# Kernel optimization log

Hardware: AMD Instinct MI355X
Metric: run time of the kernel (lower is better)

Reference implementation:

```python
import jax, jax.numpy as jnp
import numpy as np

N_RNA, N_DIS = 40000, 3000
E_EDGES, T = 600000, 10000
RNA_IN, D_FEAT, HID, EXP_D = 512, 256, 512, 256
N_EXP, HEADS = 8, 8
HD = HID // HEADS          # per-head dim inside HANConv
MHA_HD = EXP_D // HEADS    # per-head dim in cross-attention
FUSION = 2 * HID


def setup_inputs() -> dict:
    key = jax.random.key(0)
    ks = iter(jax.random.split(key, 48))
    def nrm(shape, s=0.02):
        return jax.random.normal(next(ks), shape, dtype=jnp.float32) * s
    inp = {
        "x_rna": jax.random.normal(next(ks), (N_RNA, RNA_IN), dtype=jnp.float32),
        "x_dis": jax.random.normal(next(ks), (N_DIS, D_FEAT), dtype=jnp.float32),
        "Wd": nrm((RNA_IN, D_FEAT)), "bd": jnp.zeros((RNA_IN,), jnp.float32),
        "Wp_r": nrm((HID, RNA_IN)), "bp_r": jnp.zeros((HID,), jnp.float32),
        "Wp_d": nrm((HID, RNA_IN)), "bp_d": jnp.zeros((HID,), jnp.float32),
        "a_src_rd": nrm((HEADS, HD), 0.1), "a_dst_rd": nrm((HEADS, HD), 0.1),
        "a_src_dr": nrm((HEADS, HD), 0.1), "a_dst_dr": nrm((HEADS, HD), 0.1),
        "kW": nrm((HID, HID)), "kb": jnp.zeros((HID,), jnp.float32),
        "qv": nrm((HID,), 0.1),
        "Wl": nrm((HID, HID)), "bl": jnp.zeros((HID,), jnp.float32),
        "W_exp": nrm((N_EXP, FUSION, EXP_D)), "b_exp": jnp.zeros((N_EXP, EXP_D), jnp.float32),
        "W_gate": nrm((4, HID, N_EXP)),
        "W_head": nrm((4, 2 * EXP_D, EXP_D)), "b_head": jnp.zeros((4, EXP_D), jnp.float32),
        "in_w": nrm((3 * EXP_D, EXP_D)), "in_b": jnp.zeros((3 * EXP_D,), jnp.float32),
        "out_w": nrm((EXP_D, EXP_D)), "out_b": jnp.zeros((EXP_D,), jnp.float32),
        "Wdp": nrm((EXP_D, HID)), "bdp": jnp.zeros((EXP_D,), jnp.float32),
        "ei_rd_src": jax.random.randint(next(ks), (E_EDGES,), 0, N_RNA),
        "ei_rd_dst": jax.random.randint(next(ks), (E_EDGES,), 0, N_DIS),
        "ei_dr_src": jax.random.randint(next(ks), (E_EDGES,), 0, N_DIS),
        "ei_dr_dst": jax.random.randint(next(ks), (E_EDGES,), 0, N_RNA),
        "idx_rels": jax.random.randint(next(ks), (4, T), 0, N_RNA),
    }
    return inp


def _han_edge(x_src, x_dst, ei_src, ei_dst, a_src, a_dst, n_dst):
    # x_*: [N, H, D]; GAT-style attention with softmax per destination node (PyG HANConv edge step)
    as_ = (x_src * a_src).sum(-1)                                 # [Ns, H]
    ad_ = (x_dst * a_dst).sum(-1)                                 # [Nd, H]
    alpha = jax.nn.leaky_relu(as_[ei_src] + ad_[ei_dst], 0.2)     # [E, H]
    amax = jax.ops.segment_max(alpha, ei_dst, num_segments=n_dst)
    ex = jnp.exp(alpha - amax[ei_dst])
    den = jax.ops.segment_sum(ex, ei_dst, num_segments=n_dst)
    w = ex / (den[ei_dst] + 1e-16)
    msg = x_src[ei_src] * w[:, :, None]                           # [E, H, D]
    out = jax.ops.segment_sum(msg, ei_dst, num_segments=n_dst)    # [Nd, H, D]
    return jax.nn.relu(out.reshape(n_dst, -1))


def _semantic(outs, kW, kb, qv):
    # outs: [M, N, F]; metapath-level (semantic) attention from HANConv
    s = (jnp.tanh(outs @ kW.T + kb).mean(axis=1) * qv).sum(-1)    # [M]
    beta = jax.nn.softmax(s)
    return (beta[:, None, None] * outs).sum(0)


def reference(x_rna, x_dis, Wd, bd, Wp_r, bp_r, Wp_d, bp_d,
              a_src_rd, a_dst_rd, a_src_dr, a_dst_dr,
              kW, kb, qv, Wl, bl, W_exp, b_exp, W_gate, W_head, b_head,
              in_w, in_b, out_w, out_b, Wdp, bdp,
              ei_rd_src, ei_rd_dst, ei_dr_src, ei_dr_dst, idx_rels):
    # ---- HAN encoder ----
    xd = x_dis @ Wd.T + bd                                        # disease feat -> rna_in_dim
    hr0 = (x_rna @ Wp_r.T + bp_r).reshape(N_RNA, HEADS, HD)
    hd0 = (xd @ Wp_d.T + bp_d).reshape(N_DIS, HEADS, HD)
    out_dis = _han_edge(hr0, hd0, ei_rd_src, ei_rd_dst, a_src_rd, a_dst_rd, N_DIS)
    out_rna = _han_edge(hd0, hr0, ei_dr_src, ei_dr_dst, a_src_dr, a_dst_dr, N_RNA)
    h_rna = _semantic(out_rna[None], kW, kb, qv) @ Wl.T + bl      # shared final lin
    h_dis = _semantic(out_dis[None], kW, kb, qv) @ Wl.T + bl
    # ---- MoE with per-relation gating ----
    d_global = h_dis.mean(axis=0)
    fusion = jnp.concatenate([h_rna, jnp.broadcast_to(d_global, h_rna.shape)], axis=1)  # [N, 2H]
    E = jax.nn.relu(jnp.einsum('nf,efd->ned', fusion, W_exp) + b_exp)  # [N, Nexp, Ed]
    h_t = h_rna[idx_rels]                                         # [4, T, H]
    scores = jnp.einsum('rth,rhe->rte', h_t, W_gate)              # raw gate scores (no softmax)
    u = (E[idx_rels] * scores[..., None]).sum(axis=2)             # [4, T, Ed]
    U = u.mean(axis=1)                                            # [4, Ed]
    # ---- cross attention over 4 task tokens ----
    qkv = U @ in_w.T + in_b
    q, k, v = jnp.split(qkv, 3, axis=-1)
    def heads(z):
        return z.reshape(4, HEADS, MHA_HD).transpose(1, 0, 2)     # [H, 4, dh]
    qh, kh, vh = heads(q), heads(k), heads(v)
    attn = jax.nn.softmax(jnp.einsum('htd,hsd->hts', qh, kh) / np.float32(np.sqrt(MHA_HD)), axis=-1)
    o = jnp.einsum('hts,hsd->htd', attn, vh).transpose(1, 0, 2).reshape(4, EXP_D)
    U_prime = o @ out_w.T + out_b                                 # [4, Ed]
    # ---- per-relation heads and disease scores ----
    cross = jnp.broadcast_to(U_prime[:, None, :], u.shape)
    cat = jnp.concatenate([u, cross], axis=-1)                    # [4, T, 2Ed]
    p = jax.nn.relu(jnp.einsum('rtc,rcd->rtd', cat, W_head) + b_head[:, None, :])
    d_proj = h_dis @ Wdp.T + bdp                                  # [Ndis, Ed]
    return jax.nn.sigmoid(jnp.einsum('rtd,md->rtm', p, d_proj))   # [4, T, Ndis]
```

## Files before the change

### kernel.cpp

```cpp
#include <hip/hip_runtime.h>
#include <math.h>

constexpr int NRNA = 40000;
constexpr int NDIS = 3000;
constexpr int NEDG = 600000;
constexpr int TREL = 10000;

typedef __attribute__((ext_vector_type(8))) short bh8;
typedef __attribute__((ext_vector_type(4))) float f32x4;

__device__ inline float bf2f(ushort x) {
    union { uint u; float f; } v; v.u = ((uint)x) << 16; return v.f;
}
__device__ inline ushort f2bf(float f) {
    union { float f; uint u; } v; v.f = f;
    uint u = v.u;
    uint r = (u + 0x7fffu + ((u >> 16) & 1u)) >> 16;
    return (ushort)r;
}
__device__ inline float bflo(uint w) { union { uint u; float f; } v; v.u = w << 16; return v.f; }
__device__ inline float bfhi(uint w) { union { uint u; float f; } v; v.u = w & 0xffff0000u; return v.f; }

__device__ inline void gload16(const ushort* g, ushort* l) {
    __builtin_amdgcn_global_load_lds(
        (const __attribute__((address_space(1))) unsigned int*)(const void*)g,
        (__attribute__((address_space(3))) unsigned int*)(void*)l, 16, 0, 0);
}

__device__ inline int xcd_swz(int f, int n) {
    int q = n >> 3, r = n & 7, xcd = f & 7, i = f >> 3;
    return (xcd < r) ? (xcd * (q + 1) + i) : (r * (q + 1) + (xcd - r) * q + i);
}

__global__ __launch_bounds__(256) void conv_multi(
    const float* s0, ushort* d0, const float* s1, ushort* d1,
    const float* s2, ushort* d2, const float* s3, ushort* d3,
    const float* s4, ushort* d4, const float* s5, ushort* d5,
    const float* s6, ushort* d6,
    int c0, int c1, int c2, int c3, int c4, int c5, int c6)
{
    int b = blockIdx.x;
    const float* src; ushort* dst; int base;
    if      (b < c0) { src = s0; dst = d0; base = 0;  }
    else if (b < c1) { src = s1; dst = d1; base = c0; }
    else if (b < c2) { src = s2; dst = d2; base = c1; }
    else if (b < c3) { src = s3; dst = d3; base = c2; }
    else if (b < c4) { src = s4; dst = d4; base = c3; }
    else if (b < c5) { src = s5; dst = d5; base = c4; }
    else             { src = s6; dst = d6; base = c5; }
    long g = ((long)(b - base) * 256 + threadIdx.x) * 4;
    float4 v = *(const float4*)(src + g);
    ushort4 o;
    o.x = f2bf(v.x); o.y = f2bf(v.y); o.z = f2bf(v.z); o.w = f2bf(v.w);
    *(ushort4*)(dst + g) = o;
}

__global__ __launch_bounds__(256) void transpose_bf16(
    const float* __restrict__ in, ushort* __restrict__ out,
    int R, int C, long sIn, long sOut)
{
    __shared__ float t[64][65];
    const int tid = threadIdx.x;
    const int r0 = blockIdx.y * 64, c0 = blockIdx.x * 64;
    const float* ib = in + (long)blockIdx.z * sIn;
    ushort* ob = out + (long)blockIdx.z * sOut;
#pragma unroll
    for (int k = 0; k < 16; ++k) {
        int idx = k * 256 + tid, i = idx >> 6, j = idx & 63;
        t[i][j] = ib[(long)(r0 + i) * C + c0 + j];
    }
    __syncthreads();
#pragma unroll
    for (int k = 0; k < 16; ++k) {
        int idx = k * 256 + tid, i = idx >> 6, j = idx & 63;
        ob[(long)(c0 + i) * R + r0 + j] = f2bf(t[j][i]);
    }
}

__global__ void transpose_wgate(const float* __restrict__ W, float* __restrict__ out)
{
    int g = blockIdx.x * 256 + threadIdx.x;
    int r = g >> 12, e = (g >> 9) & 7, k = g & 511;
    out[g] = W[(long)r * 4096 + (long)k * 8 + e];
}

template<int ACT, bool SWZ>
__global__ __launch_bounds__(256) void gemm_mfma(
    const ushort* __restrict__ A, const ushort* __restrict__ B,
    const float* __restrict__ bias, float* __restrict__ Cf, ushort* __restrict__ Cb,
    const int* __restrict__ idx,
    int M, int N, int K, long sA, long sB, long sBias, long sC)
{
    __shared__ ushort smem[16384];
    ushort* As = smem;
    ushort* Bs = smem + 8192;
    int bx = blockIdx.x, by = blockIdx.y;
    if (SWZ) {
        int n = gridDim.x * gridDim.y;
        int s = xcd_swz(by * gridDim.x + bx, n);
        bx = s % gridDim.x; by = s / gridDim.x;
    }
    const int bz = blockIdx.z;
    const ushort* Ab = A + (long)bz * sA;
    const ushort* Bb = B + (long)bz * sB;
    const float* biasb = bias ? (bias + (long)bz * sBias) : nullptr;
    const int row0 = by * 128, col0 = bx * 128;

    const int tid = threadIdx.x, wid = tid >> 6, lane = tid & 63;
    const int wr = wid >> 1, wc = wid & 1;

    const int lrow = lane >> 3;
    const int lk = (((lane & 7) ^ lrow) * 8);
    const ushort* ap0[4]; const ushort* bp0[4];
    ushort* la[4]; ushort* lb[4];
#pragma unroll
    for (int i = 0; i < 4; ++i) {
        int c = wid * 4 + i;
        int ra = row0 + c * 8 + lrow; ra = ra < M ? ra : M - 1;
        int rs = idx ? idx[ra] : ra;
        ap0[i] = Ab + (long)rs * K + lk;
        int cb = col0 + c * 8 + lrow; cb = cb < N ? cb : N - 1;
        bp0[i] = Bb + (long)cb * K + lk;
        la[i] = As + c * 512;
        lb[i] = Bs + c * 512;
    }

    f32x4 acc[4][4];
#pragma unroll
    for (int i = 0; i < 4; ++i)
#pragma unroll
        for (int n = 0; n < 4; ++n) acc[i][n] = (f32x4){0.f, 0.f, 0.f, 0.f};

    const int fr = lane & 15, fq = lane >> 4;
    const int sw0 = (fq ^ (fr & 7)) * 8;
    const ushort* paRow = As + (wr * 64 + fr) * 64;
    const ushort* pbRow = Bs + (wc * 64 + fr) * 64;

    for (int k0 = 0; k0 < K; k0 += 64) {
#pragma unroll
        for (int i = 0; i < 4; ++i) gload16(ap0[i] + k0, la[i]);
#pragma unroll
        for (int i = 0; i < 4; ++i) gload16(bp0[i] + k0, lb[i]);
        __syncthreads();
#pragma unroll
        for (int kk = 0; kk < 2; ++kk) {
            const int sw = kk ? (sw0 ^ 32) : sw0;
            bh8 af[4], bf[4];
#pragma unroll
            for (int i = 0; i < 4; ++i) af[i] = *(const bh8*)(paRow + i * 1024 + sw);
#pragma unroll
            for (int n = 0; n < 4; ++n) bf[n] = *(const bh8*)(pbRow + n * 1024 + sw);
#pragma unroll
            for (int i = 0; i < 4; ++i)
#pragma unroll
                for (int n = 0; n < 4; ++n)
                    acc[i][n] = __builtin_amdgcn_mfma_f32_16x16x32_bf16(af[i], bf[n], acc[i][n], 0, 0, 0);
        }
        __syncthreads();
    }

    float* cs = (float*)smem;
#pragma unroll
    for (int H = 0; H < 2; ++H) {
        if (wc == H) {
#pragma unroll
            for (int i = 0; i < 4; ++i)
#pragma unroll
                for (int n = 0; n < 4; ++n)
#pragma unroll
                    for (int r = 0; r < 4; ++r)
                        cs[(wr * 64 + i * 16 + fq * 4 + r) * 64 + n * 16 + fr] = acc[i][n][r];
        }
        __syncthreads();
#pragma unroll
        for (int it = 0; it < 8; ++it) {
            int rl = it * 16 + (tid >> 4);
            int cl = (tid & 15) * 4;
            int m = row0 + rl, col = col0 + H * 64 + cl;
            if (m < M && col < N) {
                f32x4 v = *(const f32x4*)(cs + rl * 64 + cl);
                if (biasb) {
                    float4 bv = *(const float4*)(biasb + col);
                    v[0] += bv.x; v[1] += bv.y; v[2] += bv.z; v[3] += bv.w;
                }
                if (ACT == 1) {
#pragma unroll
                    for (int q = 0; q < 4; ++q) v[q] = fmaxf(v[q], 0.f);
                } else if (ACT == 2) {
#pragma unroll
                    for (int q = 0; q < 4; ++q) v[q] = 1.f / (1.f + __expf(-v[q]));
                }
                long o = (long)bz * sC + (long)m * N + col;
                if (Cf) *(f32x4*)(Cf + o) = v;
                if (Cb) {
                    ushort4 ob;
                    ob.x = f2bf(v[0]); ob.y = f2bf(v[1]); ob.z = f2bf(v[2]); ob.w = f2bf(v[3]);
                    *(ushort4*)(Cb + o) = ob;
                }
            }
        }
        __syncthreads();
    }
}

__global__ __launch_bounds__(256) void moe_mfma(
    const ushort* __restrict__ h, const ushort* __restrict__ WexpT,
    const float* __restrict__ c_exp, const float* __restrict__ S,
    const int* __restrict__ idx, ushort* __restrict__ up)
{
    __shared__ ushort smem[24576];
    __shared__ float sS[128 * 2];
    __shared__ float sC[2 * 128];
    ushort* As  = smem;
    ushort* Bs0 = smem + 8192;
    ushort* Bs1 = smem + 16384;
    int bx = blockIdx.x, by = blockIdx.y;
    {
        int n = gridDim.x * gridDim.y;
        int s = xcd_swz(by * gridDim.x + bx, n);
        bx = s % gridDim.x; by = s / gridDim.x;
    }
    const int row0 = by * 128, col0 = bx * 128;
    const int z = blockIdx.z, e0 = z * 2;
    const int tid = threadIdx.x, wid = tid >> 6, lane = tid & 63;
    const int wr = wid >> 1, wc = wid & 1;
    constexpr int M = 4 * TREL;

    {
        int rr = tid >> 1, e = tid & 1;
        sS[tid] = S[(long)(row0 + rr) * 8 + e0 + e];
        int ee = tid >> 7, cc = tid & 127;
        sC[tid] = c_exp[(e0 + ee) * 256 + col0 + cc];
    }

    const int lrow = lane >> 3;
    const int lk = (((lane & 7) ^ lrow) * 8);
    const ushort* ap0[4]; const ushort* bp0[4];
    ushort* la[4]; ushort* lb0[4]; ushort* lb1[4];
#pragma unroll
    for (int i = 0; i < 4; ++i) {
        int c = wid * 4 + i;
        int ra = row0 + c * 8 + lrow;
        ap0[i] = h + (long)idx[ra] * 512 + lk;
        bp0[i] = WexpT + (long)(col0 + c * 8 + lrow) * 512 + (long)e0 * 131072 + lk;
        la[i]  = As  + c * 512;
        lb0[i] = Bs0 + c * 512;
        lb1[i] = Bs1 + c * 512;
    }

    const int fr = lane & 15, fq = lane >> 4;
    const int sw0 = (fq ^ (fr & 7)) * 8;
    const ushort* paRow  = As  + (wr * 64 + fr) * 64;
    const ushort* pb0Row = Bs0 + (wc * 64 + fr) * 64;
    const ushort* pb1Row = Bs1 + (wc * 64 + fr) * 64;

    f32x4 acc0[4][4], acc1[4][4];
#pragma unroll
    for (int i = 0; i < 4; ++i)
#pragma unroll
        for (int n = 0; n < 4; ++n) {
            acc0[i][n] = (f32x4){0.f, 0.f, 0.f, 0.f};
            acc1[i][n] = (f32x4){0.f, 0.f, 0.f, 0.f};
        }
    __syncthreads();

    for (int k0 = 0; k0 < 512; k0 += 64) {
#pragma unroll
        for (int i = 0; i < 4; ++i) gload16(ap0[i] + k0, la[i]);
#pragma unroll
        for (int i = 0; i < 4; ++i) gload16(bp0[i] + k0, lb0[i]);
#pragma unroll
        for (int i = 0; i < 4; ++i) gload16(bp0[i] + 131072 + k0, lb1[i]);
        __syncthreads();
#pragma unroll
        for (int kk = 0; kk < 2; ++kk) {
            const int sw = kk ? (sw0 ^ 32) : sw0;
            bh8 af[4], b0[4], b1[4];
#pragma unroll
            for (int i = 0; i < 4; ++i) af[i] = *(const bh8*)(paRow + i * 1024 + sw);
#pragma unroll
            for (int n = 0; n < 4; ++n) b0[n] = *(const bh8*)(pb0Row + n * 1024 + sw);
#pragma unroll
            for (int n = 0; n < 4; ++n) b1[n] = *(const bh8*)(pb1Row + n * 1024 + sw);
#pragma unroll
            for (int i = 0; i < 4; ++i)
#pragma unroll
                for (int n = 0; n < 4; ++n) {
                    acc0[i][n] = __builtin_amdgcn_mfma_f32_16x16x32_bf16(af[i], b0[n], acc0[i][n], 0, 0, 0);
                    acc1[i][n] = __builtin_amdgcn_mfma_f32_16x16x32_bf16(af[i], b1[n], acc1[i][n], 0, 0, 0);
                }
        }
        __syncthreads();
    }

#pragma unroll
    for (int i = 0; i < 4; ++i) {
        int rl = wr * 64 + i * 16 + fq * 4;
#pragma unroll
        for (int n = 0; n < 4; ++n) {
            int cl = wc * 64 + n * 16 + fr;
            float c0 = sC[cl], c1 = sC[128 + cl];
#pragma unroll
            for (int r = 0; r < 4; ++r) {
                float s0 = sS[(rl + r) * 2 + 0];
                float s1 = sS[(rl + r) * 2 + 1];
                acc0[i][n][r] = s0 * fmaxf(acc0[i][n][r] + c0, 0.f)
                              + s1 * fmaxf(acc1[i][n][r] + c1, 0.f);
            }
        }
    }

    float* cs = (float*)smem;
    ushort* upz = up + (long)z * M * 256;
#pragma unroll
    for (int H = 0; H < 2; ++H) {
        if (wc == H) {
#pragma unroll
            for (int i = 0; i < 4; ++i)
#pragma unroll
                for (int n = 0; n < 4; ++n)
#pragma unroll
                    for (int r = 0; r < 4; ++r)
                        cs[(wr * 64 + i * 16 + fq * 4 + r) * 64 + n * 16 + fr] = acc0[i][n][r];
        }
        __syncthreads();
#pragma unroll
        for (int it = 0; it < 8; ++it) {
            int rl = it * 16 + (tid >> 4);
            int cl = (tid & 15) * 4;
            f32x4 v = *(const f32x4*)(cs + rl * 64 + cl);
            int m = row0 + rl, col = col0 + H * 64 + cl;
            ushort4 ob;
            ob.x = f2bf(v[0]); ob.y = f2bf(v[1]); ob.z = f2bf(v[2]); ob.w = f2bf(v[3]);
            *(ushort4*)(upz + (long)m * 256 + col) = ob;
        }
        __syncthreads();
    }
}

__global__ __launch_bounds__(256) void moe_combine(const ushort* __restrict__ up,
                                                   ushort* __restrict__ u)
{
    constexpr long TOT = (long)4 * TREL * 256;
    long g = ((long)blockIdx.x * 256 + threadIdx.x) * 4;
    if (g >= TOT) return;
    float a[4] = {0.f, 0.f, 0.f, 0.f};
#pragma unroll
    for (int z = 0; z < 4; ++z) {
        ushort4 v = *(const ushort4*)(up + z * TOT + g);
        a[0] += bf2f(v.x); a[1] += bf2f(v.y); a[2] += bf2f(v.z); a[3] += bf2f(v.w);
    }
    ushort4 o;
    o.x = f2bf(a[0]); o.y = f2bf(a[1]); o.z = f2bf(a[2]); o.w = f2bf(a[3]);
    *(ushort4*)(u + g) = o;
}

__global__ void dot_heads_all(const ushort* __restrict__ xr, const ushort* __restrict__ xd,
                              const float* __restrict__ a_src_rd, const float* __restrict__ a_dst_dr,
                              const float* __restrict__ a_dst_rd, const float* __restrict__ a_src_dr,
                              float* __restrict__ as_rd, float* __restrict__ ad_dr,
                              float* __restrict__ ad_rd, float* __restrict__ as_dr)
{
    long g = (long)blockIdx.x * 256 + threadIdx.x;
    const ushort* x; const float *p1, *p2; float *o1, *o2; long gi;
    if (g < (long)NRNA * 8) {
        gi = g; x = xr; p1 = a_src_rd; p2 = a_dst_dr; o1 = as_rd; o2 = ad_dr;
    } else {
        gi = g - (long)NRNA * 8;
        if (gi >= (long)NDIS * 8) return;
        x = xd; p1 = a_dst_rd; p2 = a_src_dr; o1 = ad_rd; o2 = as_dr;
    }
    int node = (int)(gi >> 3), h = (int)(gi & 7);
    const ushort* xp = x + (long)node * 512 + h * 64;
    const float* q1 = p1 + h * 64;
    const float* q2 = p2 + h * 64;
    float s1 = 0.f, s2 = 0.f;
#pragma unroll
    for (int d = 0; d < 64; d += 8) {
        uint4 xv = *(const uint4*)(xp + d);
        float xf[8] = { bflo(xv.x), bfhi(xv.x), bflo(xv.y), bfhi(xv.y),
                        bflo(xv.z), bfhi(xv.z), bflo(xv.w), bfhi(xv.w) };
#pragma unroll
        for (int j = 0; j < 8; ++j) {
            s1 = fmaf(xf[j], q1[d + j], s1);
            s2 = fmaf(xf[j], q2[d + j], s2);
        }
    }
    o1[gi] = s1; o2[gi] = s2;
}

__global__ void hist2(const int* __restrict__ d0, int* __restrict__ deg0,
                      const int* __restrict__ d1, int* __restrict__ deg1, int E)
{
    int g = blockIdx.x * 256 + threadIdx.x;
    if (g >= E) return;
    if (blockIdx.y == 0) atomicAdd(&deg0[d0[g]], 1);
    else                 atomicAdd(&deg1[d1[g]], 1);
}

__global__ __launch_bounds__(1024) void scan_blocks2(
    const int* __restrict__ in0, int* __restrict__ tmp0, int* __restrict__ bs0, int n0,
    const int* __restrict__ in1, int* __restrict__ tmp1, int* __restrict__ bs1, int n1)
{
    const int z = blockIdx.y;
    const int* in = z ? in1 : in0;
    int* tmp = z ? tmp1 : tmp0;
    int* bsum = z ? bs1 : bs0;
    const int n = z ? n1 : n0;
    const int nb = (n + 1023) >> 10;
    if ((int)blockIdx.x >= nb) return;
    __shared__ int wsum[16];
    const int tid = threadIdx.x, lane = tid & 63, wid = tid >> 6;
    int base = blockIdx.x * 1024;
    int v = (base + tid < n) ? in[base + tid] : 0;
    int s = v;
#pragma unroll
    for (int off = 1; off < 64; off <<= 1) {
        int t = __shfl_up(s, off, 64);
        if (lane >= off) s += t;
    }
    if (lane == 63) wsum[wid] = s;
    __syncthreads();
    if (wid == 0) {
        int w = (lane < 16) ? wsum[lane] : 0;
#pragma unroll
        for (int off = 1; off < 16; off <<= 1) {
            int t = __shfl_up(w, off, 64);
            if (lane >= off) w += t;
        }
        if (lane < 16) wsum[lane] = w;
    }
    __syncthreads();
    int incl = s + ((wid == 0) ? 0 : wsum[wid - 1]);
    if (base + tid < n) tmp[base + tid] = incl;
    if (tid == 1023) bsum[blockIdx.x] = incl;
}

__global__ void scan_bsums2(int* __restrict__ bs0, int nb0, int* __restrict__ bs1, int nb1)
{
    int* bsum = blockIdx.x ? bs1 : bs0;
    int nb = blockIdx.x ? nb1 : nb0;
    int lane = threadIdx.x;
    int v = (lane < nb) ? bsum[lane] : 0;
#pragma unroll
    for (int off = 1; off < 64; off <<= 1) {
        int t = __shfl_up(v, off, 64);
        if (lane >= off) v += t;
    }
    if (lane < nb) bsum[lane] = v;
}

__global__ __launch_bounds__(1024) void scan_finish2(
    const int* __restrict__ in0, const int* __restrict__ tmp0, const int* __restrict__ bs0,
    int* __restrict__ offs0, int* __restrict__ cur0, int n0,
    const int* __restrict__ in1, const int* __restrict__ tmp1, const int* __restrict__ bs1,
    int* __restrict__ offs1, int* __restrict__ cur1, int n1)
{
    const int z = blockIdx.y;
    const int* in = z ? in1 : in0;
    const int* tmp = z ? tmp1 : tmp0;
    const int* bsum = z ? bs1 : bs0;
    int* offs = z ? offs1 : offs0;
    int* cur = z ? cur1 : cur0;
    const int n = z ? n1 : n0;
    const int nb = (n + 1023) >> 10;
    if ((int)blockIdx.x >= nb) return;
    int base = blockIdx.x * 1024;
    int i = base + threadIdx.x;
    if (i < n) {
        int pre = (blockIdx.x == 0) ? 0 : bsum[blockIdx.x - 1];
        int v = tmp[i] - in[i] + pre;
        offs[i] = v;
        cur[i] = v;
    }
    if (i == 0) offs[n] = bsum[nb - 1];
}

__global__ void scatter2(const int* __restrict__ s0, const int* __restrict__ d0,
                         int* __restrict__ c0, int* __restrict__ o0,
                         const int* __restrict__ s1, const int* __restrict__ d1,
                         int* __restrict__ c1, int* __restrict__ o1, int E)
{
    int g = blockIdx.x * 256 + threadIdx.x;
    if (g >= E) return;
    if (blockIdx.y == 0) {
        int p = atomicAdd(&c0[d0[g]], 1);
        o0[p] = s0[g];
    } else {
        int p = atomicAdd(&c1[d1[g]], 1);
        o1[p] = s1[g];
    }
}

__global__ __launch_bounds__(256) void han_wave(
    const int* __restrict__ offs, const int* __restrict__ csr_src,
    const float* __restrict__ as_, const float* __restrict__ ad_,
    const ushort* __restrict__ x_src, ushort* __restrict__ out, int nnode)
{
    __shared__ float s_ex[4][64];
    __shared__ int   s_src[4][8];
    __shared__ float s_den[4][8];
    const int w = threadIdx.x >> 6, lane = threadIdx.x & 63;
    const int node = blockIdx.x * 4 + w;
    if (node >= nnode) return;
    const int e0 = offs[node], ne = offs[node + 1] - e0;
    const int myh = lane & 7, grp = lane >> 3;
    const float my_ad = ad_[node * 8 + myh];

    float den = 0.f;
    float acc[8];
#pragma unroll
    for (int k = 0; k < 8; ++k) acc[k] = 0.f;
    const int colbase = lane * 8;

    for (int c0 = 0; c0 < ne; c0 += 8) {
        const int nc = min(8, ne - c0);
        float ex = 0.f;
        int src = 0;
        if (grp < nc) {
            src = csr_src[e0 + c0 + grp];
            float al = as_[(long)src * 8 + myh] + my_ad;
            al = al >= 0.f ? al : 0.2f * al;
            ex = __expf(al);
            den += ex;
        }
        s_ex[w][grp * 8 + myh] = ex;
        if (myh == 0) s_src[w][grp] = src;
        asm volatile("s_waitcnt lgkmcnt(0)" ::: "memory");
        for (int j = 0; j < nc; ++j) {
            float wg = s_ex[w][j * 8 + grp];
            uint4 xv = *(const uint4*)(x_src + (long)s_src[w][j] * 512 + colbase);
            acc[0] = fmaf(wg, bflo(xv.x), acc[0]);
            acc[1] = fmaf(wg, bfhi(xv.x), acc[1]);
            acc[2] = fmaf(wg, bflo(xv.y), acc[2]);
            acc[3] = fmaf(wg, bfhi(xv.y), acc[3]);
            acc[4] = fmaf(wg, bflo(xv.z), acc[4]);
            acc[5] = fmaf(wg, bfhi(xv.z), acc[5]);
            acc[6] = fmaf(wg, bflo(xv.w), acc[6]);
            acc[7] = fmaf(wg, bfhi(xv.w), acc[7]);
        }
        __builtin_amdgcn_wave_barrier();
    }

#pragma unroll
    for (int m = 8; m < 64; m <<= 1) den += __shfl_xor(den, m, 64);
    if (grp == 0) s_den[w][myh] = den;
    asm volatile("s_waitcnt lgkmcnt(0)" ::: "memory");
    float d = s_den[w][grp] + 1e-16f;

    uint4 ov;
    ov.x = (uint)f2bf(fmaxf(acc[0] / d, 0.f)) | ((uint)f2bf(fmaxf(acc[1] / d, 0.f)) << 16);
    ov.y = (uint)f2bf(fmaxf(acc[2] / d, 0.f)) | ((uint)f2bf(fmaxf(acc[3] / d, 0.f)) << 16);
    ov.z = (uint)f2bf(fmaxf(acc[4] / d, 0.f)) | ((uint)f2bf(fmaxf(acc[5] / d, 0.f)) << 16);
    ov.w = (uint)f2bf(fmaxf(acc[6] / d, 0.f)) | ((uint)f2bf(fmaxf(acc[7] / d, 0.f)) << 16);
    *(uint4*)(out + (long)node * 512 + colbase) = ov;
}

__global__ __launch_bounds__(512) void hdis_colsum_partial(const ushort* __restrict__ h_dis,
                                                           float* __restrict__ part)
{
    int c = blockIdx.x, d = threadIdx.x;
    int r0 = c * 200;
    float s = 0.f;
    for (int r = r0; r < r0 + 200; ++r) s += bf2f(h_dis[(long)r * 512 + d]);
    part[c * 512 + d] = s;
}
__global__ __launch_bounds__(512) void hdis_colsum_finish(const float* __restrict__ part,
                                                          float* __restrict__ dg)
{
    int d = threadIdx.x;
    float s = 0.f;
    for (int c = 0; c < 15; ++c) s += part[c * 512 + d];
    dg[d] = s * (1.f / NDIS);
}

__global__ void cexp_part(const float* __restrict__ dg, const float* __restrict__ W_exp,
                          float* __restrict__ part)
{
    int b = blockIdx.x;
    int e = b >> 3, ch = b & 7, d = threadIdx.x;
    const float* W = W_exp + (long)e * 262144 + (long)(512 + ch * 64) * 256 + d;
    float s = 0.f;
    for (int f = 0; f < 64; ++f) s = fmaf(dg[ch * 64 + f], W[(long)f * 256], s);
    part[b * 256 + d] = s;
}
__global__ void cexp_fin(const float* __restrict__ part, const float* __restrict__ b_exp,
                         float* __restrict__ c_exp)
{
    int e = blockIdx.x, d = threadIdx.x;
    float s = b_exp[e * 256 + d];
    for (int ch = 0; ch < 8; ++ch) s += part[(e * 8 + ch) * 256 + d];
    c_exp[e * 256 + d] = s;
}

__global__ __launch_bounds__(256) void scores2(const ushort* __restrict__ h,
                                               const float* __restrict__ WgT,
                                               const int* __restrict__ idx,
                                               float* __restrict__ S)
{
    __shared__ float sW[8 * 512];
    const int r = blockIdx.y;
    const int tid = threadIdx.x;
    for (int i = tid; i < 4096; i += 256) sW[i] = WgT[(long)r * 4096 + i];
    __syncthreads();
    int n = blockIdx.x * 256 + tid;
    if (n >= TREL) return;
    int gi = r * TREL + n;
    const ushort* hp = h + (long)idx[gi] * 512;
    float acc[8];
#pragma unroll
    for (int e = 0; e < 8; ++e) acc[e] = 0.f;
    for (int k = 0; k < 512; k += 8) {
        uint4 hv = *(const uint4*)(hp + k);
        float hf[8];
        hf[0] = bflo(hv.x); hf[1] = bfhi(hv.x); hf[2] = bflo(hv.y); hf[3] = bfhi(hv.y);
        hf[4] = bflo(hv.z); hf[5] = bfhi(hv.z); hf[6] = bflo(hv.w); hf[7] = bfhi(hv.w);
#pragma unroll
        for (int e = 0; e < 8; ++e)
#pragma unroll
            for (int j = 0; j < 8; ++j)
                acc[e] = fmaf(hf[j], sW[e * 512 + k + j], acc[e]);
    }
#pragma unroll
    for (int e = 0; e < 8; ++e) S[(long)gi * 8 + e] = acc[e];
}

__global__ void u_mean_partial(const ushort* __restrict__ u, float* __restrict__ part)
{
    int c = blockIdx.x, r = blockIdx.y, d = threadIdx.x;
    int t0 = c * 313, t1 = min(t0 + 313, TREL);
    const ushort* base = u + ((long)r * TREL) * 256 + d;
    float s = 0.f;
    for (int t = t0; t < t1; ++t) s += bf2f(base[(long)t * 256]);
    part[((long)r * 32 + c) * 256 + d] = s;
}

__global__ __launch_bounds__(256) void tail_kernel(
    const float* __restrict__ u_part,
    const float* __restrict__ in_w, const float* __restrict__ in_b,
    const float* __restrict__ out_w, const float* __restrict__ out_b,
    const float* __restrict__ W_head, const float* __restrict__ b_head,
    float* __restrict__ c_head)
{
    __shared__ float sU[4 * 256];
    __shared__ float sqkv[4 * 768];
    __shared__ float sattn[128];
    __shared__ float so[4 * 256];
    __shared__ float sUp[4 * 256];
    const int tid = threadIdx.x;

    for (int o = tid; o < 1024; o += 256) {
        int r = o >> 8, d = o & 255;
        float s = 0.f;
        for (int c = 0; c < 32; ++c) s += u_part[((long)r * 32 + c) * 256 + d];
        sU[o] = s * (1.f / TREL);
    }
    __syncthreads();

    for (int o = tid; o < 3072; o += 256) {
        int row = o / 768, col = o % 768;
        const float* w = in_w + (long)col * 256;
        const float* uu = sU + row * 256;
        float s = in_b[col];
        for (int k = 0; k < 256; ++k) s = fmaf(uu[k], w[k], s);
        sqkv[o] = s;
    }
    __syncthreads();
    if (tid < 128) {
        int h = tid >> 4, t = (tid >> 2) & 3, s2 = tid & 3;
        const float* q = sqkv + t * 768 + h * 32;
        const float* kk = sqkv + s2 * 768 + 256 + h * 32;
        float s = 0.f;
        for (int d = 0; d < 32; ++d) s += q[d] * kk[d];
        sattn[tid] = s * 0.17677669529663687f;
    }
    __syncthreads();
    if (tid < 32) {
        int base = tid * 4;
        float a0 = sattn[base], a1 = sattn[base+1], a2 = sattn[base+2], a3 = sattn[base+3];
        float m = fmaxf(fmaxf(a0, a1), fmaxf(a2, a3));
        float e0 = __expf(a0 - m), e1 = __expf(a1 - m), e2 = __expf(a2 - m), e3 = __expf(a3 - m);
        float inv = 1.f / (e0 + e1 + e2 + e3);
        sattn[base] = e0 * inv; sattn[base+1] = e1 * inv;
        sattn[base+2] = e2 * inv; sattn[base+3] = e3 * inv;
    }
    __syncthreads();
    for (int o = tid; o < 1024; o += 256) {
        int t = o >> 8, hd = o & 255, h = hd >> 5, d = hd & 31;
        const float* a = sattn + (h * 4 + t) * 4;
        float s = 0.f;
        for (int s2 = 0; s2 < 4; ++s2) s += a[s2] * sqkv[s2 * 768 + 512 + h * 32 + d];
        so[t * 256 + hd] = s;
    }
    __syncthreads();
    for (int o = tid; o < 1024; o += 256) {
        int t = o >> 8, d = o & 255;
        const float* w = out_w + (long)d * 256;
        const float* ov = so + t * 256;
        float s = out_b[d];
        for (int k = 0; k < 256; ++k) s = fmaf(ov[k], w[k], s);
        sUp[o] = s;
    }
    __syncthreads();

    for (int o = tid; o < 1024; o += 256) {
        int r = o >> 8, d = o & 255;
        const float* W = W_head + (long)r * 131072 + 65536 + d;
        const float* up = sUp + r * 256;
        float s = b_head[o];
        for (int c = 0; c < 256; ++c) s = fmaf(up[c], W[(long)c * 256], s);
        c_head[o] = s;
    }
}

extern "C" void kernel_launch(void* const* d_in, const int* in_sizes, int n_in,
                              void* d_out, int out_size, void* d_ws, size_t ws_size,
                              hipStream_t stream)
{
    (void)in_sizes; (void)n_in; (void)out_size;
    const float* x_rna    = (const float*)d_in[0];
    const float* x_dis    = (const float*)d_in[1];
    const float* Wd       = (const float*)d_in[2];
    const float* bd       = (const float*)d_in[3];
    const float* Wp_r     = (const float*)d_in[4];
    const float* bp_r     = (const float*)d_in[5];
    const float* Wp_d     = (const float*)d_in[6];
    const float* bp_d     = (const float*)d_in[7];
    const float* a_src_rd = (const float*)d_in[8];
    const float* a_dst_rd = (const float*)d_in[9];
    const float* a_src_dr = (const float*)d_in[10];
    const float* a_dst_dr = (const float*)d_in[11];
    const float* Wl       = (const float*)d_in[15];
    const float* bl       = (const float*)d_in[16];
    const float* W_exp    = (const float*)d_in[17];
    const float* b_exp    = (const float*)d_in[18];
    const float* W_gate   = (const float*)d_in[19];
    const float* W_head   = (const float*)d_in[20];
    const float* b_head   = (const float*)d_in[21];
    const float* in_w     = (const float*)d_in[22];
    const float* in_b     = (const float*)d_in[23];
    const float* out_w    = (const float*)d_in[24];
    const float* out_b    = (const float*)d_in[25];
    const float* Wdp      = (const float*)d_in[26];
    const float* bdp      = (const float*)d_in[27];
    const int* ei_rd_src  = (const int*)d_in[28];
    const int* ei_rd_dst  = (const int*)d_in[29];
    const int* ei_dr_src  = (const int*)d_in[30];
    const int* ei_dr_dst  = (const int*)d_in[31];
    const int* idx_rels   = (const int*)d_in[32];
    float* out = (float*)d_out;

    char* ws = (char*)d_ws;
    size_t off = 0;
    auto alloc = [&](size_t bytes) -> void* {
        off = (off + 255) & ~(size_t)255;
        void* p = ws + off;
        off += bytes;
        return p;
    };
    constexpr int NALL = NRNA + NDIS;
    ushort* xrb      = (ushort*)alloc((size_t)NRNA * 512 * 2);
    ushort* hr0b     = (ushort*)alloc((size_t)NRNA * 512 * 2);
    ushort* out_all  = (ushort*)alloc((size_t)(NALL + 8) * 512 * 2);
    ushort* h_all    = (ushort*)alloc((size_t)(NALL + 8) * 512 * 2);
    ushort* u_bf     = (ushort*)alloc((size_t)4 * TREL * 256 * 2);
    ushort* p_bf     = (ushort*)alloc((size_t)4 * TREL * 256 * 2);
    ushort* up_bf    = (ushort*)alloc((size_t)4 * 4 * TREL * 256 * 2);
    ushort* xdb      = (ushort*)alloc((size_t)NDIS * 256 * 2);
    ushort* xd_bf    = (ushort*)alloc((size_t)NDIS * 512 * 2);
    ushort* hd0b     = (ushort*)alloc((size_t)NDIS * 512 * 2);
    ushort* dproj_b  = (ushort*)alloc((size_t)NDIS * 256 * 2);
    ushort* Wdb    = (ushort*)alloc((size_t)512 * 256 * 2);
    ushort* Wprb   = (ushort*)alloc((size_t)512 * 512 * 2);
    ushort* Wpdb   = (ushort*)alloc((size_t)512 * 512 * 2);
    ushort* Wlb    = (ushort*)alloc((size_t)512 * 512 * 2);
    ushort* Wdpb   = (ushort*)alloc((size_t)256 * 512 * 2);
    ushort* WexpT  = (ushort*)alloc((size_t)8 * 256 * 512 * 2);
    ushort* WheadT = (ushort*)alloc((size_t)4 * 256 * 256 * 2);
    float*  WgT    = (float*)alloc((size_t)4 * 8 * 512 * 4);
    float* as_rd   = (float*)alloc((size_t)NRNA * 8 * 4);
    float* ad_rd   = (float*)alloc((size_t)NDIS * 8 * 4);
    float* as_dr   = (float*)alloc((size_t)NDIS * 8 * 4);
    float* ad_dr   = (float*)alloc((size_t)NRNA * 8 * 4);
    float* S       = (float*)alloc((size_t)4 * TREL * 8 * 4);
    float* dg_part = (float*)alloc((size_t)16 * 512 * 4);
    float* dg      = (float*)alloc((size_t)512 * 4);
    float* c_exp   = (float*)alloc((size_t)8 * 256 * 4);
    float* ce_part = (float*)alloc((size_t)64 * 256 * 4);
    float* u_part  = (float*)alloc((size_t)4 * 32 * 256 * 4);
    float* c_head  = (float*)alloc((size_t)4 * 256 * 4);
    int* deg_all  = (int*)alloc((size_t)(NDIS + NRNA) * 4);
    int* deg_rd = deg_all, * deg_dr = deg_all + NDIS;
    int* offs_rd = (int*)alloc((size_t)(NDIS + 1) * 4);
    int* cur_rd  = (int*)alloc((size_t)NDIS * 4);
    int* csr_rd  = (int*)alloc((size_t)NEDG * 4);
    int* offs_dr = (int*)alloc((size_t)(NRNA + 1) * 4);
    int* cur_dr  = (int*)alloc((size_t)NRNA * 4);
    int* csr_dr  = (int*)alloc((size_t)NEDG * 4);
    int* tmp_rd  = (int*)alloc((size_t)NDIS * 4);
    int* tmp_dr  = (int*)alloc((size_t)NRNA * 4);
    int* bs_rd   = (int*)alloc((size_t)64 * 4);
    int* bs_dr   = (int*)alloc((size_t)64 * 4);
    if (off > ws_size) return;

    ushort* out_rna = out_all;
    ushort* out_dis = out_all + (size_t)NRNA * 512;
    ushort* h_rna   = h_all;
    ushort* h_dis   = h_all + (size_t)NRNA * 512;

    const dim3 blk(256);

    conv_multi<<<dim3(21774), blk, 0, stream>>>(
        x_rna, xrb, x_dis, xdb, Wd, Wdb, Wp_r, Wprb, Wp_d, Wpdb, Wl, Wlb, Wdp, Wdpb,
        20000, 20750, 20878, 21134, 21390, 21646, 21774);
    transpose_bf16<<<dim3(4, 8, 8), blk, 0, stream>>>(W_exp, WexpT, 512, 256,
                                                      (long)1024 * 256, (long)256 * 512);
    transpose_bf16<<<dim3(4, 4, 4), blk, 0, stream>>>(W_head, WheadT, 256, 256,
                                                      (long)512 * 256, (long)256 * 256);
    transpose_wgate<<<dim3(64), blk, 0, stream>>>(W_gate, WgT);

    gemm_mfma<0,false><<<dim3(4, 24), blk, 0, stream>>>(
        xdb, Wdb, bd, nullptr, xd_bf, nullptr, NDIS, 512, 256, 0, 0, 0, 0);
    gemm_mfma<0,true><<<dim3(4, 313), blk, 0, stream>>>(
        xrb, Wprb, bp_r, nullptr, hr0b, nullptr, NRNA, 512, 512, 0, 0, 0, 0);
    gemm_mfma<0,false><<<dim3(4, 24), blk, 0, stream>>>(
        xd_bf, Wpdb, bp_d, nullptr, hd0b, nullptr, NDIS, 512, 512, 0, 0, 0, 0);

    dot_heads_all<<<dim3(((NRNA + NDIS) * 8 + 255) / 256), blk, 0, stream>>>(
        hr0b, hd0b, a_src_rd, a_dst_dr, a_dst_rd, a_src_dr, as_rd, ad_dr, ad_rd, as_dr);

    hipMemsetAsync(deg_all, 0, (size_t)(NDIS + NRNA) * 4, stream);
    hist2<<<dim3((NEDG + 255) / 256, 2), blk, 0, stream>>>(ei_rd_dst, deg_rd, ei_dr_dst, deg_dr, NEDG);
    scan_blocks2<<<dim3(40, 2), dim3(1024), 0, stream>>>(deg_rd, tmp_rd, bs_rd, NDIS,
                                                         deg_dr, tmp_dr, bs_dr, NRNA);
    scan_bsums2<<<dim3(2), dim3(64), 0, stream>>>(bs_rd, 3, bs_dr, 40);
    scan_finish2<<<dim3(40, 2), dim3(1024), 0, stream>>>(deg_rd, tmp_rd, bs_rd, offs_rd, cur_rd, NDIS,
                                                         deg_dr, tmp_dr, bs_dr, offs_dr, cur_dr, NRNA);
    scatter2<<<dim3((NEDG + 255) / 256, 2), blk, 0, stream>>>(
        ei_rd_src, ei_rd_dst, cur_rd, csr_rd, ei_dr_src, ei_dr_dst, cur_dr, csr_dr, NEDG);

    han_wave<<<dim3((NDIS + 3) / 4), blk, 0, stream>>>(offs_rd, csr_rd, as_rd, ad_rd, hr0b, out_dis, NDIS);
    han_wave<<<dim3(NRNA / 4), blk, 0, stream>>>(offs_dr, csr_dr, as_dr, ad_dr, hd0b, out_rna, NRNA);

    gemm_mfma<0,true><<<dim3(4, (NALL + 127) / 128), blk, 0, stream>>>(
        out_all, Wlb, bl, nullptr, h_all, nullptr, NALL, 512, 512, 0, 0, 0, 0);

    hdis_colsum_partial<<<dim3(15), dim3(512), 0, stream>>>(h_dis, dg_part);
    hdis_colsum_finish<<<dim3(1), dim3(512), 0, stream>>>(dg_part, dg);
    cexp_part<<<dim3(64), blk, 0, stream>>>(dg, W_exp, ce_part);
    cexp_fin<<<dim3(8), blk, 0, stream>>>(ce_part, b_exp, c_exp);
    scores2<<<dim3(40, 4), blk, 0, stream>>>(h_rna, WgT, idx_rels, S);

    moe_mfma<<<dim3(2, 320, 4), blk, 0, stream>>>(h_rna, WexpT, c_exp, S, idx_rels, up_bf);
    moe_combine<<<dim3(10240), blk, 0, stream>>>(up_bf, u_bf);

    u_mean_partial<<<dim3(32, 4), blk, 0, stream>>>(u_bf, u_part);
    tail_kernel<<<dim3(1), blk, 0, stream>>>(u_part, in_w, in_b, out_w, out_b,
                                             W_head, b_head, c_head);

    gemm_mfma<1,false><<<dim3(2, 79, 4), blk, 0, stream>>>(
        u_bf, WheadT, c_head, nullptr, p_bf, nullptr, TREL, 256, 256,
        (long)TREL * 256, 65536, 256, (long)TREL * 256);

    gemm_mfma<0,false><<<dim3(2, 24), blk, 0, stream>>>(
        h_dis, Wdpb, bdp, nullptr, dproj_b, nullptr, NDIS, 256, 512, 0, 0, 0, 0);

    gemm_mfma<2,true><<<dim3(24, 320), blk, 0, stream>>>(
        p_bf, dproj_b, nullptr, out, nullptr, nullptr, 4 * TREL, NDIS, 256, 0, 0, 0, 0);
}
```

Measured before the change: 1.266 ms.

## Fuse relation-head GEMM with disease-score GEMM and sigmoid into one kernel

Replaces two launches with a single kernel, one block per 128-row tile per relation. The first launch computed the per-relation head projection with ReLU and wrote it to memory; the second multiplied it by the disease projection and applied a sigmoid. The new kernel computes the ReLU'd head tile into LDS, then loops over all 24 disease-column tiles using that resident tile as the A operand. This removes the write and re-read of the intermediate p tensor and one launch. In exchange, the grid drops to 316 large-LDS blocks, which limits occupancy and latency hiding. Loads are not double-buffered, and the large fp32 output is written with scalar rather than vectorised stores.

```diff
diff --git a/kernel.cpp b/kernel.cpp
--- a/kernel.cpp
+++ b/kernel.cpp
@@ -200,6 +200,149 @@
             }
         }
         __syncthreads();
+    }
+}
+
+__global__ __launch_bounds__(256) void pout_fused(
+    const ushort* __restrict__ u, const ushort* __restrict__ WheadT,
+    const float* __restrict__ c_head, const ushort* __restrict__ dproj,
+    float* __restrict__ out)
+{
+    __shared__ ushort smem[40960];
+    ushort* P  = smem;
+    ushort* Bs = smem + 32768;
+    const int rel = blockIdx.y;
+    const int row0 = blockIdx.x * 128;
+    const int tid = threadIdx.x, wid = tid >> 6, lane = tid & 63;
+    const int wr = wid >> 1, wc = wid & 1;
+    const int fr = lane & 15, fq = lane >> 4;
+    const int lrow = lane >> 3;
+    const int lk = ((lane & 7) ^ lrow) * 8;
+    const int sw0 = (fq ^ (fr & 7)) * 8;
+
+    const ushort* ub = u + (long)rel * TREL * 256;
+#pragma unroll
+    for (int i = 0; i < 4; ++i) {
+        int c = wid * 4 + i;
+        int ra = row0 + c * 8 + lrow; ra = ra < TREL ? ra : TREL - 1;
+        const ushort* src = ub + (long)ra * 256 + lk;
+        ushort* dst = P + c * 512;
+#pragma unroll
+        for (int t = 0; t < 4; ++t)
+            gload16(src + t * 64, dst + t * 8192);
+    }
+
+    f32x4 acc2[2][4][4];
+#pragma unroll
+    for (int h = 0; h < 2; ++h)
+#pragma unroll
+        for (int i = 0; i < 4; ++i)
+#pragma unroll
+            for (int n = 0; n < 4; ++n) acc2[h][i][n] = (f32x4){0.f, 0.f, 0.f, 0.f};
+
+    const ushort* whb = WheadT + (long)rel * 65536;
+    const ushort* paRow = P + (wr * 64 + fr) * 64;
+    const ushort* pbRow = Bs + (wc * 64 + fr) * 64;
+
+#pragma unroll
+    for (int h = 0; h < 2; ++h) {
+        for (int k0 = 0; k0 < 4; ++k0) {
+#pragma unroll
+            for (int i = 0; i < 4; ++i) {
+                int c = wid * 4 + i;
+                gload16(whb + (long)(h * 128 + c * 8 + lrow) * 256 + k0 * 64 + lk,
+                        Bs + c * 512);
+            }
+            __syncthreads();
+#pragma unroll
+            for (int kk = 0; kk < 2; ++kk) {
+                const int sw = kk ? (sw0 ^ 32) : sw0;
+                bh8 af[4], bf[4];
+#pragma unroll
+                for (int i = 0; i < 4; ++i) af[i] = *(const bh8*)(paRow + k0 * 8192 + i * 1024 + sw);
+#pragma unroll
+                for (int n = 0; n < 4; ++n) bf[n] = *(const bh8*)(pbRow + n * 1024 + sw);
+#pragma unroll
+                for (int i = 0; i < 4; ++i)
+#pragma unroll
+                    for (int n = 0; n < 4; ++n)
+                        acc2[h][i][n] = __builtin_amdgcn_mfma_f32_16x16x32_bf16(af[i], bf[n], acc2[h][i][n], 0, 0, 0);
+            }
+            __syncthreads();
+        }
+    }
+
+    const float* chb = c_head + rel * 256;
+#pragma unroll
+    for (int h = 0; h < 2; ++h) {
+#pragma unroll
+        for (int n = 0; n < 4; ++n) {
+            int cg = h * 128 + wc * 64 + n * 16 + fr;
+            float cb = chb[cg];
+            int tile = cg >> 6, c6 = cg & 63;
+            int ssrc = c6 >> 3, coff = c6 & 7;
+#pragma unroll
+            for (int i = 0; i < 4; ++i) {
+#pragma unroll
+                for (int r = 0; r < 4; ++r) {
+                    int ml = wr * 64 + i * 16 + fq * 4 + r;
+                    float v = fmaxf(acc2[h][i][n][r] + cb, 0.f);
+                    P[tile * 8192 + ml * 64 + ((ssrc ^ (ml & 7)) * 8) + coff] = f2bf(v);
+                }
+            }
+        }
+    }
+    __syncthreads();
+
+    const long orow0 = (long)rel * TREL + row0;
+    for (int nt = 0; nt < 24; ++nt) {
+        const int col0 = nt * 128;
+        f32x4 acc[4][4];
+#pragma unroll
+        for (int i = 0; i < 4; ++i)
+#pragma unroll
+            for (int n = 0; n < 4; ++n) acc[i][n] = (f32x4){0.f, 0.f, 0.f, 0.f};
+
+        for (int k0 = 0; k0 < 4; ++k0) {
+#pragma unroll
+            for (int i = 0; i < 4; ++i) {
+                int c = wid * 4 + i;
+                int cb = col0 + c * 8 + lrow; cb = cb < NDIS ? cb : NDIS - 1;
+                gload16(dproj + (long)cb * 256 + k0 * 64 + lk, Bs + c * 512);
+            }
+            __syncthreads();
+#pragma unroll
+            for (int kk = 0; kk < 2; ++kk) {
+                const int sw = kk ? (sw0 ^ 32) : sw0;
+                bh8 af[4], bf[4];
+#pragma unroll
+                for (int i = 0; i < 4; ++i) af[i] = *(const bh8*)(paRow + k0 * 8192 + i * 1024 + sw);
+#pragma unroll
+                for (int n = 0; n < 4; ++n) bf[n] = *(const bh8*)(pbRow + n * 1024 + sw);
+#pragma unroll
+                for (int i = 0; i < 4; ++i)
+#pragma unroll
+                    for (int n = 0; n < 4; ++n)
+                        acc[i][n] = __builtin_amdgcn_mfma_f32_16x16x32_bf16(af[i], bf[n], acc[i][n], 0, 0, 0);
+            }
+            __syncthreads();
+        }
+
+#pragma unroll
+        for (int i = 0; i < 4; ++i) {
+#pragma unroll
+            for (int r = 0; r < 4; ++r) {
+                int mrel = row0 + wr * 64 + i * 16 + fq * 4 + r;
+                if (mrel >= TREL) continue;
+#pragma unroll
+                for (int n = 0; n < 4; ++n) {
+                    int col = col0 + wc * 64 + n * 16 + fr;
+                    if (col < NDIS)
+                        out[(orow0 + (long)(wr * 64 + i * 16 + fq * 4 + r)) * NDIS + col] =
+                            1.f / (1.f + __expf(-acc[i][n][r]));
+                }
+            }
+        }
     }
 }
 
@@ -802,6 +945,7 @@
     int* bs_rd   = (int*)alloc((size_t)64 * 4);
     int* bs_dr   = (int*)alloc((size_t)64 * 4);
     if (off > ws_size) return;
+    (void)p_bf;
 
     ushort* out_rna = out_all;
     ushort* out_dis = out_all + (size_t)NRNA * 512;
@@ -858,13 +1002,8 @@
     tail_kernel<<<dim3(1), blk, 0, stream>>>(u_part, in_w, in_b, out_w, out_b,
                                              W_head, b_head, c_head);
 
-    gemm_mfma<1,false><<<dim3(2, 79, 4), blk, 0, stream>>>(
-        u_bf, WheadT, c_head, nullptr, p_bf, nullptr, TREL, 256, 256,
-        (long)TREL * 256, 65536, 256, (long)TREL * 256);
-
     gemm_mfma<0,false><<<dim3(2, 24), blk, 0, stream>>>(
         h_dis, Wdpb, bdp, nullptr, dproj_b, nullptr, NDIS, 256, 512, 0, 0, 0, 0);
 
-    gemm_mfma<2,true><<<dim3(24, 320), blk, 0, stream>>>(
-        p_bf, dproj_b, nullptr, out, nullptr, nullptr, 4 * TREL, NDIS, 256, 0, 0, 0, 0);
-}
+    pout_fused<<<dim3(79, 4), blk, 0, stream>>>(u_bf, WheadT, c_head, dproj_b, out);
+}
```

Result: slower. 1.422 ms (+12.3%).
